# Optimization experiments

Hardware: AMD Instinct MI355X
Metric: run time of the kernel (lower is better)

Reference implementation:

```python
import jax, jax.numpy as jnp
import numpy as np

MUL_S, MUL_V = 16, 8   # 16x0e + 8x1o -> input dim 16 + 8*3 = 40
N = 500_000
SQRT3 = 3.0 ** 0.5

# e3nn normalize2mom: scale act so E[act(x)^2]=1 for x~N(0,1)
def _norm2mom(act):
    xs = np.linspace(-12.0, 12.0, 200001)
    pdf = np.exp(-0.5 * xs * xs) / np.sqrt(2.0 * np.pi)
    m2 = np.trapz(act(xs) ** 2 * pdf, xs)
    return float(1.0 / np.sqrt(m2))

SILU_C = _norm2mom(lambda x: x / (1.0 + np.exp(-x)))
SIG_C = _norm2mom(lambda x: 1.0 / (1.0 + np.exp(-x)))

# e3nn path normalization (irrep_normalization='component', path_normalization='element')
C_SC = (1.0 / (MUL_S * MUL_S + MUL_V * MUL_V)) ** 0.5          # 0e outputs (scalars & gates)
C_V = (3.0 / (2 * MUL_S * MUL_V)) ** 0.5                        # 1o output (gated)


def setup_inputs() -> dict:
    key = jax.random.key(0)
    ks = jax.random.split(key, 7)
    return {
        "x": jax.random.normal(ks[0], (N, MUL_S + 3 * MUL_V), dtype=jnp.float32),
        "W_ss0": jax.random.normal(ks[1], (MUL_S, MUL_S, MUL_S), dtype=jnp.float32),
        "W_vv0": jax.random.normal(ks[2], (MUL_V, MUL_V, MUL_S), dtype=jnp.float32),
        "W_ss1": jax.random.normal(ks[3], (MUL_S, MUL_S, MUL_V), dtype=jnp.float32),
        "W_vv1": jax.random.normal(ks[4], (MUL_V, MUL_V, MUL_V), dtype=jnp.float32),
        "W_sv": jax.random.normal(ks[5], (MUL_S, MUL_V, MUL_V), dtype=jnp.float32),
        "W_vs": jax.random.normal(ks[6], (MUL_V, MUL_S, MUL_V), dtype=jnp.float32),
    }


def reference(x, W_ss0, W_vv0, W_ss1, W_vv1, W_sv, W_vs):
    # split irreps: scalars [N,16], vectors [N,8,3]
    s = x[:, :MUL_S]
    v = x[:, MUL_S:].reshape(-1, MUL_V, 3)

    # FullyConnectedTensorProduct(x, x) -> scalars(16x0e) + gates(8x0e) + gated(8x1o)
    # wigner_3j(0,0,0)=1 ; (1,1,0)=(0,1,1)=(1,0,1)=I/sqrt(3)
    scal = C_SC * (
        jnp.einsum('zu,zv,uvw->zw', s, s, W_ss0)
        + jnp.einsum('zui,zvi,uvw->zw', v, v, W_vv0) / SQRT3
    )
    gates_pre = C_SC * (
        jnp.einsum('zu,zv,uvw->zw', s, s, W_ss1)
        + jnp.einsum('zui,zvi,uvw->zw', v, v, W_vv1) / SQRT3
    )
    gated = (C_V / SQRT3) * (
        jnp.einsum('zu,zvi,uvw->zwi', s, v, W_sv)
        + jnp.einsum('zui,zv,uvw->zwi', v, s, W_vs)
    )

    # Gate: normalized silu on even scalars, normalized sigmoid gates * gated vectors
    out_s = SILU_C * jax.nn.silu(scal)                 # [N,16]
    g = SIG_C * jax.nn.sigmoid(gates_pre)              # [N,8]
    out_v = g[:, :, None] * gated                      # [N,8,3]
    return jnp.concatenate([out_s, out_v.reshape(-1, MUL_V * 3)], axis=1)
```

## Files before the change

### kernel.cpp

```cpp
#include <hip/hip_runtime.h>
#include <math.h>

#define NPTS 200001

typedef _Float16 f16;
typedef f16 f16x2 __attribute__((ext_vector_type(2)));
typedef f16 f16x8 __attribute__((ext_vector_type(8)));
typedef float f32x16 __attribute__((ext_vector_type(16)));

__global__ void prep(const float* __restrict__ wss0, const float* __restrict__ wvv0,
                     const float* __restrict__ wss1, const float* __restrict__ wvv1,
                     const float* __restrict__ wsv,  const float* __restrict__ wvs,
                     float* __restrict__ partials,
                     f16* __restrict__ b1, f16* __restrict__ b2)
{
    const int b = blockIdx.x;
    const int t = threadIdx.x;
    if (b < 4) {
        float ls = 0.f, lg = 0.f;
        for (int i = b * 256 + t; i < NPTS; i += 1024) {
            float xv  = -12.0f + 24.0f * ((float)i / 200000.0f);
            float pdf = __expf(-0.5f * xv * xv) * 0.39894228040143267794f;
            float sg  = 1.0f / (1.0f + __expf(-xv));
            float si  = xv * sg;
            float wt  = (i == 0 || i == NPTS - 1) ? 0.5f : 1.0f;
            ls = fmaf(wt * si * si, pdf, ls);
            lg = fmaf(wt * sg * sg, pdf, lg);
        }
        __shared__ float r1[256], r2[256];
        r1[t] = ls; r2[t] = lg;
        __syncthreads();
        for (int st = 128; st > 0; st >>= 1) {
            if (t < st) { r1[t] += r1[t + st]; r2[t] += r2[t + st]; }
            __syncthreads();
        }
        if (t == 0) { partials[b] = r1[0]; partials[4 + b] = r2[0]; }
    } else {
        const int gid = (b - 4) * 256 + t;
        const float CSC  = 0.05590169943749474241f;
        const float CSC3 = 0.05590169943749474241f / 1.7320508075688772935f;
        if (gid < 14336) {
            const int e = gid;
            const int tt   = e >> 9;
            const int lane = (e >> 3) & 63;
            const int j    = e & 7;
            const int n    = lane & 31;
            const int hf   = lane >> 5;
            const int k    = tt * 16 + hf * 8 + j;
            float val = 0.f;
            if (k < 256) {
                const int u = k >> 4, t16 = k & 15;
                if (n < 16)      val = CSC * wss0[(u * 16 + t16) * 16 + n];
                else if (n < 24) val = CSC * wss1[(u * 16 + t16) * 8 + (n - 16)];
            } else {
                const int kk = k - 256;
                const int r8 = (kk >> 3) & 7, c8 = kk & 7;
                if (n < 16)      val = CSC3 * wvv0[(r8 * 8 + c8) * 16 + n];
                else if (n < 24) val = CSC3 * wvv1[(r8 * 8 + c8) * 8 + (n - 16)];
            }
            b1[e] = (f16)val;
        } else if (gid < 18432) {
            const int e = gid - 14336;
            const int tt   = e >> 9;
            const int lane = (e >> 3) & 63;
            const int j    = e & 7;
            const int n    = lane & 31;
            const int hf   = lane >> 5;
            const int k    = tt * 16 + hf * 8 + j;
            const int a = k >> 3, bb = k & 7;
            float val = 0.f;
            if (n < 8)
                val = 0.0625f * (wsv[(a * 8 + bb) * 8 + n] + wvs[(bb * 16 + a) * 8 + n]);
            b2[e] = (f16)val;
        }
    }
}

__global__ __launch_bounds__(256, 2) void seg_main(
    const float* __restrict__ x,
    const f16* __restrict__ b1,
    const f16* __restrict__ b2,
    const float* __restrict__ partials,
    float* __restrict__ out, int n, int nchunks)
{
    const int lane = threadIdx.x & 63;
    const int wid  = threadIdx.x >> 6;
    const int col  = lane & 31;
    const int hf   = lane >> 5;

    f16x8 B1[28];
    const f16x8* b1v = (const f16x8*)b1;
#pragma unroll
    for (int t = 0; t < 28; ++t) B1[t] = b1v[t * 64 + lane];
    f16x8 B2f[8];
    const f16x8* b2v = (const f16x8*)b2;
#pragma unroll
    for (int t = 0; t < 8; ++t) B2f[t] = b2v[t * 64 + lane];

    const float dx = 24.0f / 200000.0f;
    const float silu_c = rsqrtf((partials[0] + partials[1] + partials[2] + partials[3]) * dx);
    const float sig_c  = rsqrtf((partials[4] + partials[5] + partials[6] + partials[7]) * dx);

    for (int chunk = blockIdx.x * 4 + wid; chunk < nchunks; chunk += gridDim.x * 4) {
        const int row  = chunk * 32 + col;
        const int lrow = (row < n) ? row : (n - 1);

        f16x2 s2[8];
        f16x2 vc[3][4];
        {
            float xr[40] __attribute__((aligned(16)));
            const float4* p4 = (const float4*)(x + (size_t)lrow * 40);
#pragma unroll
            for (int q = 0; q < 10; ++q) ((float4*)xr)[q] = p4[q];
#pragma unroll
            for (int a = 0; a < 8; ++a) { s2[a].x = (f16)xr[2 * a]; s2[a].y = (f16)xr[2 * a + 1]; }
#pragma unroll
            for (int i = 0; i < 3; ++i)
#pragma unroll
                for (int m = 0; m < 4; ++m) {
                    vc[i][m].x = (f16)xr[16 + 3 * (2 * m) + i];
                    vc[i][m].y = (f16)xr[16 + 3 * (2 * m + 1) + i];
                }
        }
        f16x2 shp[4];
#pragma unroll
        for (int m = 0; m < 4; ++m) shp[m] = hf ? s2[4 + m] : s2[m];

        union { f16x2 h[4]; f16x8 v; } A;
        f32x16 acc1;
#pragma unroll
        for (int r = 0; r < 16; ++r) acc1[r] = 0.f;

#pragma unroll
        for (int t = 0; t < 16; ++t) {
            f16 sv = (t & 1) ? s2[t >> 1].y : s2[t >> 1].x;
            f16x2 su2; su2.x = sv; su2.y = sv;
#pragma unroll
            for (int m = 0; m < 4; ++m) A.h[m] = su2 * shp[m];
            acc1 = __builtin_amdgcn_mfma_f32_32x32x16_f16(A.v, B1[t], acc1, 0, 0, 0);
        }
#pragma unroll
        for (int tt = 0; tt < 12; ++tt) {
            const int i   = tt >> 2;
            const int ttm = tt & 3;
            f16x2 pr = vc[i][ttm];
            f16 sv = hf ? pr.y : pr.x;
            f16x2 su2; su2.x = sv; su2.y = sv;
#pragma unroll
            for (int m = 0; m < 4; ++m) A.h[m] = su2 * vc[i][m];
            acc1 = __builtin_amdgcn_mfma_f32_32x32x16_f16(A.v, B1[16 + tt], acc1, 0, 0, 0);
        }

        float gall[16];
#pragma unroll
        for (int r = 0; r < 16; ++r) {
            float val = acc1[r];
            float sgm = 1.0f / (1.0f + __expf(-val));
            gall[r] = sig_c * sgm;
            const int z  = (r & 3) + 8 * (r >> 2) + 4 * hf;
            const int zr = chunk * 32 + z;
            if (col < 16 && zr < n)
                out[(size_t)zr * 40 + col] = silu_c * val * sgm;
        }
        float gm[16];
#pragma unroll
        for (int r = 0; r < 16; ++r) gm[r] = __shfl(gall[r], (lane + 16) & 63, 64);

#pragma unroll
        for (int i = 0; i < 3; ++i) {
            f32x16 acc2;
#pragma unroll
            for (int r = 0; r < 16; ++r) acc2[r] = 0.f;
#pragma unroll
            for (int t2 = 0; t2 < 8; ++t2) {
                f16x2 pr = s2[t2];
                f16 sv = hf ? pr.y : pr.x;
                f16x2 su2; su2.x = sv; su2.y = sv;
#pragma unroll
                for (int m = 0; m < 4; ++m) A.h[m] = su2 * vc[i][m];
                acc2 = __builtin_amdgcn_mfma_f32_32x32x16_f16(A.v, B2f[t2], acc2, 0, 0, 0);
            }
            if (col < 8) {
#pragma unroll
                for (int r = 0; r < 16; ++r) {
                    const int z  = (r & 3) + 8 * (r >> 2) + 4 * hf;
                    const int zr = chunk * 32 + z;
                    if (zr < n)
                        out[(size_t)zr * 40 + 16 + col * 3 + i] = gm[r] * acc2[r];
                }
            }
        }
    }
}

extern "C" void kernel_launch(void* const* d_in, const int* in_sizes, int n_in,
                              void* d_out, int out_size, void* d_ws, size_t ws_size,
                              hipStream_t stream)
{
    (void)n_in; (void)out_size; (void)ws_size;
    const float* x    = (const float*)d_in[0];
    const float* wss0 = (const float*)d_in[1];
    const float* wvv0 = (const float*)d_in[2];
    const float* wss1 = (const float*)d_in[3];
    const float* wvv1 = (const float*)d_in[4];
    const float* wsv  = (const float*)d_in[5];
    const float* wvs  = (const float*)d_in[6];
    float* out = (float*)d_out;
    const int n = in_sizes[0] / 40;
    const int nchunks = (n + 31) / 32;

    char* ws = (char*)d_ws;
    float* partials = (float*)(ws + 0);
    f16*   b1       = (f16*)(ws + 1024);
    f16*   b2       = (f16*)(ws + 30720);

    hipLaunchKernelGGL(prep, dim3(76), dim3(256), 0, stream,
                       wss0, wvv0, wss1, wvv1, wsv, wvs, partials, b1, b2);
    hipLaunchKernelGGL(seg_main, dim3(512), dim3(256), 0, stream,
                       x, b1, b2, partials, out, n, nchunks);
}
```

Before: 217.0 us.

## Stage MFMA B fragments in LDS, prefetch next chunk, raise occupancy

```diff
diff --git a/kernel.cpp b/kernel.cpp
--- a/kernel.cpp
+++ b/kernel.cpp
@@ -76,7 +76,7 @@
     }
 }
 
-__global__ __launch_bounds__(256, 2) void seg_main(
+__global__ __launch_bounds__(256, 3) void seg_main(
     const float* __restrict__ x,
     const f16* __restrict__ b1,
     const f16* __restrict__ b2,
@@ -88,40 +88,58 @@
     const int col  = lane & 31;
     const int hf   = lane >> 5;
 
-    f16x8 B1[28];
-    const f16x8* b1v = (const f16x8*)b1;
-#pragma unroll
-    for (int t = 0; t < 28; ++t) B1[t] = b1v[t * 64 + lane];
-    f16x8 B2f[8];
-    const f16x8* b2v = (const f16x8*)b2;
-#pragma unroll
-    for (int t = 0; t < 8; ++t) B2f[t] = b2v[t * 64 + lane];
+    __shared__ float4 ldsB[2304];
+    {
+        const float4* b1v4 = (const float4*)b1;
+        const float4* b2v4 = (const float4*)b2;
+#pragma unroll
+        for (int i = 0; i < 7; ++i) ldsB[i * 256 + threadIdx.x] = b1v4[i * 256 + threadIdx.x];
+#pragma unroll
+        for (int i = 0; i < 2; ++i) ldsB[1792 + i * 256 + threadIdx.x] = b2v4[i * 256 + threadIdx.x];
+    }
+    __syncthreads();
+    const f16x8* Bf = (const f16x8*)ldsB;
 
     const float dx = 24.0f / 200000.0f;
     const float silu_c = rsqrtf((partials[0] + partials[1] + partials[2] + partials[3]) * dx);
     const float sig_c  = rsqrtf((partials[4] + partials[5] + partials[6] + partials[7]) * dx);
 
-    for (int chunk = blockIdx.x * 4 + wid; chunk < nchunks; chunk += gridDim.x * 4) {
+    const int stride = gridDim.x * 4;
+    int chunk = blockIdx.x * 4 + wid;
+
+    float xr[40] __attribute__((aligned(16)));
+    if (chunk < nchunks) {
         const int row  = chunk * 32 + col;
         const int lrow = (row < n) ? row : (n - 1);
-
+        const float4* p4 = (const float4*)(x + (size_t)lrow * 40);
+#pragma unroll
+        for (int q = 0; q < 10; ++q) ((float4*)xr)[q] = p4[q];
+    }
+
+    for (; chunk < nchunks; chunk += stride) {
         f16x2 s2[8];
         f16x2 vc[3][4];
+#pragma unroll
+        for (int a = 0; a < 8; ++a) { s2[a].x = (f16)xr[2 * a]; s2[a].y = (f16)xr[2 * a + 1]; }
+#pragma unroll
+        for (int i = 0; i < 3; ++i)
+#pragma unroll
+            for (int m = 0; m < 4; ++m) {
+                vc[i][m].x = (f16)xr[16 + 6 * m + i];
+                vc[i][m].y = (f16)xr[16 + 6 * m + 3 + i];
+            }
+
         {
-            float xr[40] __attribute__((aligned(16)));
-            const float4* p4 = (const float4*)(x + (size_t)lrow * 40);
-#pragma unroll
-            for (int q = 0; q < 10; ++q) ((float4*)xr)[q] = p4[q];
-#pragma unroll
-            for (int a = 0; a < 8; ++a) { s2[a].x = (f16)xr[2 * a]; s2[a].y = (f16)xr[2 * a + 1]; }
-#pragma unroll
-            for (int i = 0; i < 3; ++i)
-#pragma unroll
-                for (int m = 0; m < 4; ++m) {
-                    vc[i][m].x = (f16)xr[16 + 3 * (2 * m) + i];
-                    vc[i][m].y = (f16)xr[16 + 3 * (2 * m + 1) + i];
-                }
-        }
+            const int nxt = chunk + stride;
+            if (nxt < nchunks) {
+                const int row  = nxt * 32 + col;
+                const int lrow = (row < n) ? row : (n - 1);
+                const float4* p4 = (const float4*)(x + (size_t)lrow * 40);
+#pragma unroll
+                for (int q = 0; q < 10; ++q) ((float4*)xr)[q] = p4[q];
+            }
+        }
+
         f16x2 shp[4];
 #pragma unroll
         for (int m = 0; m < 4; ++m) shp[m] = hf ? s2[4 + m] : s2[m];
@@ -137,7 +155,7 @@
             f16x2 su2; su2.x = sv; su2.y = sv;
 #pragma unroll
             for (int m = 0; m < 4; ++m) A.h[m] = su2 * shp[m];
-            acc1 = __builtin_amdgcn_mfma_f32_32x32x16_f16(A.v, B1[t], acc1, 0, 0, 0);
+            acc1 = __builtin_amdgcn_mfma_f32_32x32x16_f16(A.v, Bf[t * 64 + lane], acc1, 0, 0, 0);
         }
 #pragma unroll
         for (int tt = 0; tt < 12; ++tt) {
@@ -148,7 +166,7 @@
             f16x2 su2; su2.x = sv; su2.y = sv;
 #pragma unroll
             for (int m = 0; m < 4; ++m) A.h[m] = su2 * vc[i][m];
-            acc1 = __builtin_amdgcn_mfma_f32_32x32x16_f16(A.v, B1[16 + tt], acc1, 0, 0, 0);
+            acc1 = __builtin_amdgcn_mfma_f32_32x32x16_f16(A.v, Bf[(16 + tt) * 64 + lane], acc1, 0, 0, 0);
         }
 
         float gall[16];
@@ -164,7 +182,8 @@
         }
         float gm[16];
 #pragma unroll
-        for (int r = 0; r < 16; ++r) gm[r] = __shfl(gall[r], (lane + 16) & 63, 64);
+        for (int r = 0; r < 16; ++r)
+            gm[r] = __int_as_float(__builtin_amdgcn_ds_swizzle(__float_as_int(gall[r]), 0x401F));
 
 #pragma unroll
         for (int i = 0; i < 3; ++i) {
@@ -178,7 +197,7 @@
                 f16x2 su2; su2.x = sv; su2.y = sv;
 #pragma unroll
                 for (int m = 0; m < 4; ++m) A.h[m] = su2 * vc[i][m];
-                acc2 = __builtin_amdgcn_mfma_f32_32x32x16_f16(A.v, B2f[t2], acc2, 0, 0, 0);
+                acc2 = __builtin_amdgcn_mfma_f32_32x32x16_f16(A.v, Bf[1792 + t2 * 64 + lane], acc2, 0, 0, 0);
             }
             if (col < 8) {
 #pragma unroll
@@ -214,8 +233,11 @@
     f16*   b1       = (f16*)(ws + 1024);
     f16*   b2       = (f16*)(ws + 30720);
 
+    int grid = (nchunks + 3) / 4;
+    if (grid > 1024) grid = 1024;
+
     hipLaunchKernelGGL(prep, dim3(76), dim3(256), 0, stream,
                        wss0, wvv0, wss1, wvv1, wsv, wvs, partials, b1, b2);
-    hipLaunchKernelGGL(seg_main, dim3(512), dim3(256), 0, stream,
+    hipLaunchKernelGGL(seg_main, dim3(grid), dim3(256), 0, stream,
                        x, b1, b2, partials, out, n, nchunks);
 }
```

Measured after the change: 302.8 us. 1.4x slower.
